# Performance work log

Measured on AMD Instinct MI355X. Metric: run time of the kernel, lower is better.

Reference implementation:

```python
import jax, jax.numpy as jnp
import numpy as np

N_NODES = 100000
N_EDGES = 1600000
N_GRAPHS = 128


def _gru(x, w_ih, w_hh, b_ih, b_hh):
    # x: [N, T, D]; torch nn.GRU single layer, batch_first
    N, T, D = x.shape
    H = w_hh.shape[1]
    gi = jnp.einsum('ntd,gd->ntg', x, w_ih) + b_ih  # [N, T, 3H]

    def step(h, g_t):
        gh = h @ w_hh.T + b_hh
        i_r, i_z, i_n = jnp.split(g_t, 3, axis=-1)
        h_r, h_z, h_n = jnp.split(gh, 3, axis=-1)
        r = jax.nn.sigmoid(i_r + h_r)
        z = jax.nn.sigmoid(i_z + h_z)
        n = jnp.tanh(i_n + r * h_n)
        h_new = (1 - z) * n + z * h
        return h_new, None

    h0 = jnp.zeros((N, H), x.dtype)
    h, _ = jax.lax.scan(step, h0, jnp.swapaxes(gi, 0, 1))
    return h  # [N, H]


def _gat(x, W, att_src, att_dst, bias, src, dst, num_nodes, concat):
    # PyG GATConv: linear, per-head attention logits, segment softmax over dst, scatter-add
    H, C = att_src.shape
    xs = (x @ W).reshape(num_nodes, H, C)
    a_src = (xs * att_src).sum(-1)  # [N, H]
    a_dst = (xs * att_dst).sum(-1)  # [N, H]
    e = jax.nn.leaky_relu(a_src[src] + a_dst[dst], 0.2)  # [E, H]
    emax = jax.ops.segment_max(e, dst, num_segments=num_nodes)
    ee = jnp.exp(e - emax[dst])
    denom = jax.ops.segment_sum(ee, dst, num_segments=num_nodes)
    alpha = ee / (denom[dst] + 1e-16)
    msg = xs[src] * alpha[:, :, None]  # [E, H, C]
    out = jax.ops.segment_sum(msg, dst, num_segments=num_nodes)  # [N, H, C]
    if concat:
        out = out.reshape(num_nodes, H * C)
    else:
        out = out.mean(axis=1)
    return out + bias


def setup_inputs() -> dict:
    key = jax.random.key(0)
    ks = jax.random.split(key, 20)
    s = 0.05
    inp = {
        'x': jax.random.normal(ks[0], (N_NODES, 8, 128), jnp.float32),
        'edge_index': jax.random.randint(ks[1], (2, N_EDGES), 0, N_NODES, jnp.int32),
        'batch': jnp.sort(jax.random.randint(ks[2], (N_NODES,), 0, N_GRAPHS, jnp.int32)),
        'num_graphs': N_GRAPHS,
        'gru_w_ih': jax.random.normal(ks[3], (192, 128)) * s,
        'gru_w_hh': jax.random.normal(ks[4], (192, 64)) * s,
        'gru_b_ih': jax.random.normal(ks[5], (192,)) * s,
        'gru_b_hh': jax.random.normal(ks[6], (192,)) * s,
        'W1': jax.random.normal(ks[7], (64, 256)) * s,
        'att_src1': jax.random.normal(ks[8], (4, 64)) * s,
        'att_dst1': jax.random.normal(ks[9], (4, 64)) * s,
        'b1': jax.random.normal(ks[10], (256,)) * s,
        'W2': jax.random.normal(ks[11], (256, 64)) * s,
        'att_src2': jax.random.normal(ks[12], (1, 64)) * s,
        'att_dst2': jax.random.normal(ks[13], (1, 64)) * s,
        'b2': jax.random.normal(ks[14], (64,)) * s,
        'attn_w': jax.random.normal(ks[15], (64, 1)) * s,
        'attn_b': jax.random.normal(ks[16], (1,)) * s,
        'fc_w': jax.random.normal(ks[17], (64, 10)) * s,
        'fc_b': jax.random.normal(ks[18], (10,)) * s,
    }
    return inp


def reference(x, edge_index, batch, num_graphs, gru_w_ih, gru_w_hh, gru_b_ih, gru_b_hh,
              W1, att_src1, att_dst1, b1, W2, att_src2, att_dst2, b2,
              attn_w, attn_b, fc_w, fc_b):
    N = x.shape[0]
    h = _gru(x, gru_w_ih, gru_w_hh, gru_b_ih, gru_b_hh)  # [N, 64]
    # GATConv default add_self_loops=True
    loops = jnp.arange(N, dtype=edge_index.dtype)
    src = jnp.concatenate([edge_index[0], loops])
    dst = jnp.concatenate([edge_index[1], loops])
    h = jax.nn.relu(_gat(h, W1, att_src1, att_dst1, b1, src, dst, N, concat=True))   # [N, 256]
    h = jax.nn.relu(_gat(h, W2, att_src2, att_dst2, b2, src, dst, N, concat=False))  # [N, 64]
    # softmax over dim=1 of [N,1] -> all ones (faithful to the original code)
    aw = jax.nn.softmax(h @ attn_w + attn_b, axis=1)  # [N, 1]
    weighted = aw * h
    sums = jax.ops.segment_sum(weighted, batch, num_segments=num_graphs)  # [G, 64]
    counts = jax.ops.segment_sum(jnp.ones((N,), h.dtype), batch, num_segments=num_graphs)
    graph_feat = sums / jnp.maximum(counts, 1.0)[:, None]
    out = graph_feat @ fc_w + fc_b
    return jax.nn.log_softmax(out, axis=-1)
```

## Files before the change

kernel.cpp:

```cpp
#include <hip/hip_runtime.h>
#include <stdint.h>


typedef __attribute__((ext_vector_type(8))) short short8;
typedef __attribute__((ext_vector_type(4))) float f32x4;
typedef __attribute__((ext_vector_type(2))) float f32x2;
typedef __attribute__((ext_vector_type(2))) unsigned int u32x2;
typedef __attribute__((ext_vector_type(4))) unsigned int u32x4;

__device__ __forceinline__ unsigned short f2bf(float f) {
    unsigned u = __float_as_uint(f);
    u += 0x7FFFu + ((u >> 16) & 1u);
    return (unsigned short)(u >> 16);
}
__device__ __forceinline__ float bf2f(unsigned short h) {
    return __uint_as_float(((unsigned)h) << 16);
}
__device__ __forceinline__ unsigned cvtpk(float lo, float hi) {
    unsigned r;
    asm("v_cvt_pk_bf16_f32 %0, %1, %2" : "=v"(r) : "v"(lo), "v"(hi));
    return r;
}
__device__ __forceinline__ unsigned short f2bfq(float v) {
    unsigned r;
    asm("v_cvt_pk_bf16_f32 %0, %1, %1" : "=v"(r) : "v"(v));
    return (unsigned short)r;
}
__device__ __forceinline__ float lrelu(float x) { return x > 0.f ? x : 0.2f * x; }
__device__ __forceinline__ float fsig(float a) {
    return __builtin_amdgcn_rcpf(1.f + __expf(-a));
}
__device__ __forceinline__ float ftanh(float a) {
    return 2.f * __builtin_amdgcn_rcpf(1.f + __expf(-2.f * a)) - 1.f;
}
__device__ __forceinline__ unsigned enc4fp8(float a, float b, float c, float d) {
    unsigned r = __builtin_amdgcn_cvt_pk_fp8_f32(a, b, 0, false);
    r = __builtin_amdgcn_cvt_pk_fp8_f32(c, d, r, true);
    return r;
}
__device__ __forceinline__ unsigned char enc1fp8(float v) {
    return (unsigned char)(__builtin_amdgcn_cvt_pk_fp8_f32(v, v, 0, false) & 0xff);
}

__device__ void pack_body(const float* __restrict__ src, unsigned short* __restrict__ dst,
                          int K, int NCOL, int ldsrc, int transposed, int blk, int tid) {
    int id = blk * 256 + tid;
    int KT = K >> 5;
    int nfrag = (NCOL >> 4) * KT;
    if (id >= nfrag * 64) return;
    int l = id & 63;
    int f = id >> 6;
    int kt = f % KT, ct = f / KT;
    int col = ct * 16 + (l & 15);
    int kbase = kt * 32 + ((l >> 4) << 3);
#pragma unroll
    for (int i = 0; i < 8; i++) {
        int k = kbase + i;
        float v = transposed ? src[(size_t)col * ldsrc + k] : src[(size_t)k * ldsrc + col];
        dst[((size_t)f * 64 + l) * 8 + i] = f2bf(v);
    }
}
__device__ void packv_body(const float* __restrict__ W, const float* __restrict__ avs,
                           const float* __restrict__ avd, unsigned short* __restrict__ dst,
                           int K, int H, int ldW, int blk, int tid) {
    int id = blk * 256 + tid;
    int KT = K >> 5;
    if (id >= KT * 64) return;
    int l = id & 63, f = id >> 6;
    int col = l & 15;
    int kbase = f * 32 + ((l >> 4) << 3);
    for (int i = 0; i < 8; i++) {
        int k = kbase + i;
        float val = 0.f;
        if (col < 2 * H) {
            int h = col >> 1;
            const float* av = (col & 1) ? avd : avs;
            for (int c = 0; c < 64; c++) val += W[(size_t)k * ldW + h * 64 + c] * av[h * 64 + c];
        }
        dst[((size_t)f * 64 + l) * 8 + i] = f2bf(val);
    }
}
__global__ void k_prep(const float* w_ih, const float* w_hh, const float* W1, const float* W2,
                       const float* as1, const float* ad1, const float* as2, const float* ad2,
                       const float* b1,
                       unsigned short* p_gi, unsigned short* p_gh,
                       unsigned short* p_w1, unsigned short* p_w2,
                       unsigned short* p_v1, unsigned short* p_v2,
                       float* b1p) {
    int b = blockIdx.x, tid = threadIdx.x;
    if (b < 12)      pack_body(w_ih, p_gi, 128, 192, 128, 1, b, tid);
    else if (b < 18) pack_body(w_hh, p_gh, 64, 192, 64, 1, b - 12, tid);
    else if (b < 26) pack_body(W1, p_w1, 64, 256, 256, 0, b - 18, tid);
    else if (b < 34) pack_body(W2, p_w2, 256, 64, 64, 0, b - 26, tid);
    else if (b < 35) packv_body(W1, as1, ad1, p_v1, 64, 4, 256, b - 34, tid);
    else if (b < 37) packv_body(W2, as2, ad2, p_v2, 256, 1, 64, b - 35, tid);
    else {
        int o = tid;
        int p = (o & 0xC0) | ((o & 15) << 2) | ((o >> 4) & 3);
        b1p[p] = b1[o];
    }
}

__launch_bounds__(256, 2)
__global__ void k_gru(const float* __restrict__ x,
                      const unsigned short* __restrict__ pgi,
                      const unsigned short* __restrict__ pgh,
                      const float* __restrict__ b_ih, const float* __restrict__ b_hh,
                      unsigned short* __restrict__ h1, int N) {
    __shared__ unsigned short x_pack[4 * 4 * 64 * 8];
    __shared__ unsigned short h_pack[4 * 2 * 64 * 8];

    const int tid = threadIdx.x;
    const int w = tid >> 6;
    const int l = tid & 63;
    const int row0 = blockIdx.x * 64;

    short8 wgi[3][4], wgh[3][2];
#pragma unroll
    for (int g = 0; g < 3; g++) {
        int ctg = g * 4 + w;
#pragma unroll
        for (int kt = 0; kt < 4; kt++)
            wgi[g][kt] = *(const short8*)(pgi + ((size_t)(ctg * 4 + kt) * 64 + l) * 8);
#pragma unroll
        for (int kt = 0; kt < 2; kt++)
            wgh[g][kt] = *(const short8*)(pgh + ((size_t)(ctg * 2 + kt) * 64 + l) * 8);
    }
    const int j = (w << 4) + (l & 15);
    const float bs_r = b_ih[j] + b_hh[j];
    const float bs_z = b_ih[64 + j] + b_hh[64 + j];
    const float bi_n = b_ih[128 + j], bh_n = b_hh[128 + j];

    f32x4 hreg[4];
    const f32x4 z4 = {0.f, 0.f, 0.f, 0.f};
#pragma unroll
    for (int m = 0; m < 4; m++) hreg[m] = z4;

    const int sr = tid >> 2, sub = tid & 3;
    const int snode = min(row0 + sr, N - 1);
    const int slane = (sr & 15) | (sub << 4);
    const int sm = sr >> 4;
    const float* xbase = x + (size_t)snode * 1024;

    float4 pre[8];
#pragma unroll
    for (int it = 0; it < 4; it++) {
        int d0 = it * 32 + sub * 8;
        pre[2 * it] = *(const float4*)(xbase + d0);
        pre[2 * it + 1] = *(const float4*)(xbase + d0 + 4);
    }

    for (int t = 0; t < 8; t++) {
        u32x4 pk[4];
#pragma unroll
        for (int it = 0; it < 4; it++) {
            float4 va = pre[2 * it], vb = pre[2 * it + 1];
            u32x4 p;
            p[0] = cvtpk(va.x, va.y); p[1] = cvtpk(va.z, va.w);
            p[2] = cvtpk(vb.x, vb.y); p[3] = cvtpk(vb.z, vb.w);
            pk[it] = p;
        }
        if (t > 0) {
#pragma unroll
            for (int m = 0; m < 4; m++)
#pragma unroll
                for (int q = 0; q < 4; q++) {
                    int rl = ((l >> 4) << 2) + q;
                    int lane2 = rl | (((j >> 3) & 3) << 4);
                    h_pack[((m * 2 + (j >> 5)) * 64 + lane2) * 8 + (j & 7)] = f2bfq(hreg[m][q]);
                }
        }
#pragma unroll
        for (int it = 0; it < 4; it++)
            *(u32x4*)&x_pack[((sm * 4 + it) * 64 + slane) * 8] = pk[it];
        __syncthreads();

        if (t < 7) {
            const float* xp = xbase + (t + 1) * 128;
#pragma unroll
            for (int it = 0; it < 4; it++) {
                int d0 = it * 32 + sub * 8;
                pre[2 * it] = *(const float4*)(xp + d0);
                pre[2 * it + 1] = *(const float4*)(xp + d0 + 4);
            }
        }

        f32x4 agi[4][3], aghn[4];
#pragma unroll
        for (int m = 0; m < 4; m++) {
            agi[m][0] = z4; agi[m][1] = z4; agi[m][2] = z4; aghn[m] = z4;
        }

#pragma unroll
        for (int m = 0; m < 4; m++) {
#pragma unroll
            for (int kt = 0; kt < 4; kt++) {
                short8 a = *(const short8*)&x_pack[((m * 4 + kt) * 64 + l) * 8];
#pragma unroll
                for (int g = 0; g < 3; g++)
                    agi[m][g] = __builtin_amdgcn_mfma_f32_16x16x32_bf16(a, wgi[g][kt], agi[m][g], 0, 0, 0);
            }
            if (t > 0) {
#pragma unroll
                for (int kt = 0; kt < 2; kt++) {
                    short8 a = *(const short8*)&h_pack[((m * 2 + kt) * 64 + l) * 8];
                    agi[m][0] = __builtin_amdgcn_mfma_f32_16x16x32_bf16(a, wgh[0][kt], agi[m][0], 0, 0, 0);
                    agi[m][1] = __builtin_amdgcn_mfma_f32_16x16x32_bf16(a, wgh[1][kt], agi[m][1], 0, 0, 0);
                    aghn[m]   = __builtin_amdgcn_mfma_f32_16x16x32_bf16(a, wgh[2][kt], aghn[m], 0, 0, 0);
                }
            }
        }
#pragma unroll
        for (int m = 0; m < 4; m++) {
#pragma unroll
            for (int q = 0; q < 4; q++) {
                float rr = fsig(agi[m][0][q] + bs_r);
                float zz = fsig(agi[m][1][q] + bs_z);
                float hn = aghn[m][q] + bh_n;
                float nn = ftanh(agi[m][2][q] + bi_n + rr * hn);
                hreg[m][q] = nn + zz * (hreg[m][q] - nn);
            }
        }
        __syncthreads();
    }
#pragma unroll
    for (int m = 0; m < 4; m++)
#pragma unroll
        for (int q = 0; q < 4; q++) {
            int node = row0 + (m << 4) + ((l >> 4) << 2) + q;
            if (node < N) h1[(size_t)node * 64 + j] = f2bfq(hreg[m][q]);
        }
}

__launch_bounds__(256, 2)
__global__ void k_gemm1(const unsigned short* __restrict__ A,
                        const unsigned short* __restrict__ packB,
                        const unsigned short* __restrict__ pv1,
                        unsigned char* __restrict__ Cf,
                        float* __restrict__ aS, float* __restrict__ aD, int N) {
    constexpr int KT = 2, CPW = 4;
    __shared__ unsigned short a_pack[4 * KT * 64 * 8];

    const int tid = threadIdx.x, w = tid >> 6, l = tid & 63;
    const int row0 = blockIdx.x * 64;

    short8 bf[CPW][KT];
#pragma unroll
    for (int ci = 0; ci < CPW; ci++)
#pragma unroll
        for (int kt = 0; kt < KT; kt++)
            bf[ci][kt] = *(const short8*)(packB + ((size_t)((w * CPW + ci) * KT + kt) * 64 + l) * 8);

    const int sr = tid >> 2, sub = tid & 3;
    const int snode = min(row0 + sr, N - 1);
    const unsigned short* ap = A + (size_t)snode * 64;
#pragma unroll
    for (int it = 0; it < KT; it++) {
        int d0 = it * 32 + sub * 8;
        short8 v = *(const short8*)(ap + d0);
        *(short8*)&a_pack[(((sr >> 4) * KT + it) * 64 + ((sr & 15) | (sub << 4))) * 8] = v;
    }
    __syncthreads();

    const f32x4 z4 = {0.f, 0.f, 0.f, 0.f};
    f32x4 acc[4][CPW];
#pragma unroll
    for (int m = 0; m < 4; m++)
#pragma unroll
        for (int ci = 0; ci < CPW; ci++) acc[m][ci] = z4;

#pragma unroll
    for (int m = 0; m < 4; m++)
#pragma unroll
        for (int kt = 0; kt < KT; kt++) {
            short8 a = *(const short8*)&a_pack[((m * KT + kt) * 64 + l) * 8];
#pragma unroll
            for (int ci = 0; ci < CPW; ci++)
                acc[m][ci] = __builtin_amdgcn_mfma_f32_16x16x32_bf16(a, bf[ci][kt], acc[m][ci], 0, 0, 0);
        }

    f32x4 acce = z4;
#pragma unroll
    for (int kt = 0; kt < KT; kt++) {
        short8 be = *(const short8*)(pv1 + ((size_t)kt * 64 + l) * 8);
        short8 a = *(const short8*)&a_pack[((w * KT + kt) * 64 + l) * 8];
        acce = __builtin_amdgcn_mfma_f32_16x16x32_bf16(a, be, acce, 0, 0, 0);
    }
    int colE = l & 15;
    if (colE < 8) {
        int h = colE >> 1;
#pragma unroll
        for (int q = 0; q < 4; q++) {
            int node = row0 + (w << 4) + ((l >> 4) << 2) + q;
            if (node < N) {
                if (colE & 1) aD[node * 4 + h] = acce[q];
                else          aS[node * 4 + h] = acce[q];
            }
        }
    }

    const int lc = l & 15;
#pragma unroll
    for (int m = 0; m < 4; m++)
#pragma unroll
        for (int q = 0; q < 4; q++) {
            int node = row0 + (m << 4) + ((l >> 4) << 2) + q;
            if (node < N) {
                unsigned d = enc4fp8(acc[m][0][q], acc[m][1][q], acc[m][2][q], acc[m][3][q]);
                *(unsigned*)(Cf + (size_t)node * 256 + w * 64 + lc * 4) = d;
            }
        }
}

__launch_bounds__(256, 2)
__global__ void k_gemm2(const unsigned short* __restrict__ A,
                        const unsigned short* __restrict__ packB,
                        const unsigned short* __restrict__ pv2,
                        unsigned char* __restrict__ Cf,
                        float* __restrict__ aS, float* __restrict__ aD, int N) {
    constexpr int KT = 8;
    __shared__ unsigned short a_pack[4 * KT * 64 * 8];

    const int tid = threadIdx.x, w = tid >> 6, l = tid & 63;
    const int row0 = blockIdx.x * 64;

    short8 bf[KT];
#pragma unroll
    for (int kt = 0; kt < KT; kt++)
        bf[kt] = *(const short8*)(packB + ((size_t)(w * KT + kt) * 64 + l) * 8);

    const int sr = tid >> 2, sub = tid & 3;
    const int snode = min(row0 + sr, N - 1);
    const unsigned short* ap = A + (size_t)snode * 256;
#pragma unroll
    for (int it = 0; it < KT; it++) {
        int d0 = it * 32 + sub * 8;
        short8 v = *(const short8*)(ap + d0);
        *(short8*)&a_pack[(((sr >> 4) * KT + it) * 64 + ((sr & 15) | (sub << 4))) * 8] = v;
    }
    __syncthreads();

    const f32x4 z4 = {0.f, 0.f, 0.f, 0.f};
    f32x4 acc[4];
#pragma unroll
    for (int m = 0; m < 4; m++) acc[m] = z4;

#pragma unroll
    for (int m = 0; m < 4; m++)
#pragma unroll
        for (int kt = 0; kt < KT; kt++) {
            short8 a = *(const short8*)&a_pack[((m * KT + kt) * 64 + l) * 8];
            acc[m] = __builtin_amdgcn_mfma_f32_16x16x32_bf16(a, bf[kt], acc[m], 0, 0, 0);
        }

    f32x4 acce = z4;
#pragma unroll
    for (int kt = 0; kt < KT; kt++) {
        short8 be = *(const short8*)(pv2 + ((size_t)kt * 64 + l) * 8);
        short8 a = *(const short8*)&a_pack[((w * KT + kt) * 64 + l) * 8];
        acce = __builtin_amdgcn_mfma_f32_16x16x32_bf16(a, be, acce, 0, 0, 0);
    }
    int colE = l & 15;
    if (colE < 2) {
#pragma unroll
        for (int q = 0; q < 4; q++) {
            int node = row0 + (w << 4) + ((l >> 4) << 2) + q;
            if (node < N) {
                if (colE) aD[node] = acce[q];
                else      aS[node] = acce[q];
            }
        }
    }

    int colw = w * 16 + (l & 15);
#pragma unroll
    for (int m = 0; m < 4; m++)
#pragma unroll
        for (int q = 0; q < 4; q++) {
            int node = row0 + (m << 4) + ((l >> 4) << 2) + q;
            if (node < N) Cf[(size_t)node * 64 + colw] = enc1fp8(acc[m][q]);
        }
}

__global__ void k_deg(const int* __restrict__ dst, int* __restrict__ deg, int E) {
    int i = blockIdx.x * blockDim.x + threadIdx.x;
    if (i < E) atomicAdd(&deg[dst[i]], 1);
}
__global__ void k_scan1(const int* __restrict__ deg, int* __restrict__ inc,
                        int* __restrict__ bsum, int N) {
    __shared__ int wsum[16];
    int tid = threadIdx.x;
    int i = blockIdx.x * 1024 + tid;
    int v = (i < N) ? deg[i] : 0;
    int lane = tid & 63, wv = tid >> 6;
    int s = v;
#pragma unroll
    for (int d = 1; d < 64; d <<= 1) {
        int t = __shfl_up(s, d);
        if (lane >= d) s += t;
    }
    if (lane == 63) wsum[wv] = s;
    __syncthreads();
    if (tid == 0) {
        int run = 0;
#pragma unroll
        for (int k = 0; k < 16; k++) { int t = wsum[k]; wsum[k] = run; run += t; }
        bsum[blockIdx.x] = run;
    }
    __syncthreads();
    s += wsum[wv];
    if (i < N) inc[i] = s;
}
__global__ void k_scan2(int* __restrict__ bsum, int nb) {
    __shared__ int w0tot;
    int tid = threadIdx.x;
    int v = (tid < nb) ? bsum[tid] : 0;
    int lane = tid & 63, wv = tid >> 6;
    int s = v;
#pragma unroll
    for (int d = 1; d < 64; d <<= 1) {
        int t = __shfl_up(s, d);
        if (lane >= d) s += t;
    }
    if (tid == 63) w0tot = s;
    __syncthreads();
    int ex = s - v + (wv ? w0tot : 0);
    if (tid < nb) bsum[tid] = ex;
}
__global__ void k_scan3(const int* __restrict__ inc, const int* __restrict__ bsum,
                        int* __restrict__ off, int* __restrict__ cursor, int N) {
    int i = blockIdx.x * blockDim.x + threadIdx.x;
    if (i < N) { off[i + 1] = inc[i] + bsum[i >> 10]; cursor[i] = 0; }
    if (i == 0) off[0] = 0;
}
__global__ void k_fill(const int* __restrict__ srcv, const int* __restrict__ dstv,
                       const int* __restrict__ off, int* __restrict__ cursor,
                       int* __restrict__ ssrc, int E) {
    int i = blockIdx.x * blockDim.x + threadIdx.x;
    if (i < E) {
        int d = dstv[i];
        int pos = off[d] + atomicAdd(&cursor[d], 1);
        ssrc[pos] = srcv[i];
    }
}

__global__ void k_agg1(const unsigned char* __restrict__ xs,
                       const float* __restrict__ a_s, const float* __restrict__ a_d,
                       const int* __restrict__ off, const int* __restrict__ ssrc,
                       const float* __restrict__ b1p,
                       unsigned short* __restrict__ out, int N) {
    int v = blockIdx.x * 4 + (threadIdx.x >> 6);
    if (v >= N) return;
    const int l = threadIdx.x & 63;
    const int eq = l >> 4;
    const int cq = l & 15;
    const int H = cq >> 2;
    const float adv = a_d[v * 4 + H];
    const int beg = off[v], end = off[v + 1];
    const int cnt = end - beg;

    float s_;
    float ac[16];
    {
        u32x4 xv = *(const u32x4*)(xs + (size_t)v * 256 + cq * 16);
        float pv = (eq == 0) ? __expf(lrelu(a_s[v * 4 + H] + adv)) : 0.f;
        s_ = pv;
#pragma unroll
        for (int wd = 0; wd < 4; wd++) {
            f32x2 lo = __builtin_amdgcn_cvt_pk_f32_fp8(xv[wd], false);
            f32x2 hi = __builtin_amdgcn_cvt_pk_f32_fp8(xv[wd], true);
            ac[wd * 4 + 0] = pv * lo[0]; ac[wd * 4 + 1] = pv * lo[1];
            ac[wd * 4 + 2] = pv * hi[0]; ac[wd * 4 + 3] = pv * hi[1];
        }
    }

#define AG1_LOAD(S, POS) { int pp = min((POS) + eq, cl); int uu = ssrc[beg + pp]; \
        aa##S = a_s[uu * 4 + H]; x##S = *(const u32x4*)(xs + (size_t)uu * 256 + cq * 16); }
#define AG1_PROC(S) { float p = __expf(lrelu(aa##S + adv)); s_ += p; \
        _Pragma("unroll") for (int wd = 0; wd < 4; wd++) { \
            f32x2 lo = __builtin_amdgcn_cvt_pk_f32_fp8(x##S[wd], false); \
            f32x2 hi = __builtin_amdgcn_cvt_pk_f32_fp8(x##S[wd], true); \
            ac[wd * 4 + 0] += p * lo[0]; ac[wd * 4 + 1] += p * lo[1]; \
            ac[wd * 4 + 2] += p * hi[0]; ac[wd * 4 + 3] += p * hi[1]; } }

    float aa0 = 0.f, aa1 = 0.f, aa2 = 0.f;
    u32x4 x0 = {0, 0, 0, 0}, x1 = {0, 0, 0, 0}, x2 = {0, 0, 0, 0};
    int k = 0;
    if (cnt > 0) {
        const int cl = cnt - 1;
        AG1_LOAD(0, 0) AG1_LOAD(1, 4) AG1_LOAD(2, 8)
        for (; k + 12 <= cnt; k += 12) {
            AG1_PROC(0) AG1_LOAD(0, k + 12)
            AG1_PROC(1) AG1_LOAD(1, k + 16)
            AG1_PROC(2) AG1_LOAD(2, k + 20)
        }
        if (k + eq < cnt)     AG1_PROC(0)
        if (k + 4 + eq < cnt) AG1_PROC(1)
        if (k + 8 + eq < cnt) AG1_PROC(2)
    }
#undef AG1_LOAD
#undef AG1_PROC

#pragma unroll
    for (int msk = 16; msk < 64; msk <<= 1) {
        s_ += __shfl_xor(s_, msk);
#pragma unroll
        for (int i = 0; i < 16; i++) ac[i] += __shfl_xor(ac[i], msk);
    }

    if (eq == 0) {
        float inv = __builtin_amdgcn_rcpf(s_ + 1e-16f);
        float bp[16];
#pragma unroll
        for (int i = 0; i < 4; i++)
            *(float4*)&bp[i * 4] = *(const float4*)(b1p + cq * 16 + i * 4);
#pragma unroll
        for (int b = 0; b < 4; b++) {
            float r0 = fmaxf(ac[b]      * inv + bp[b],      0.f);
            float r1 = fmaxf(ac[4 + b]  * inv + bp[4 + b],  0.f);
            float r2 = fmaxf(ac[8 + b]  * inv + bp[8 + b],  0.f);
            float r3 = fmaxf(ac[12 + b] * inv + bp[12 + b], 0.f);
            u32x2 o;
            o[0] = cvtpk(r0, r1); o[1] = cvtpk(r2, r3);
            *(u32x2*)(out + (size_t)v * 256 + H * 64 + b * 16 + (cq & 3) * 4) = o;
        }
    }
}

__global__ void k_agg2(const unsigned char* __restrict__ xs,
                       const float* __restrict__ a_s, const float* __restrict__ a_d,
                       const int* __restrict__ off, const int* __restrict__ ssrc,
                       const float* __restrict__ bias,
                       float* __restrict__ out, int N) {
    int v = blockIdx.x * 4 + (threadIdx.x >> 6);
    if (v >= N) return;
    const int l = threadIdx.x & 63;
    const int eo = l >> 3;
    const int cq = l & 7;
    const int c0 = cq * 8;
    const float adv = a_d[v];
    const int beg = off[v], end = off[v + 1];
    const int cnt = end - beg;

    float s_;
    float ac[8];
    {
        u32x2 xv = *(const u32x2*)(xs + (size_t)v * 64 + c0);
        float pv = (eo == 0) ? __expf(lrelu(a_s[v] + adv)) : 0.f;
        s_ = pv;
#pragma unroll
        for (int wd = 0; wd < 2; wd++) {
            f32x2 lo = __builtin_amdgcn_cvt_pk_f32_fp8(xv[wd], false);
            f32x2 hi = __builtin_amdgcn_cvt_pk_f32_fp8(xv[wd], true);
            ac[wd * 4 + 0] = pv * lo[0]; ac[wd * 4 + 1] = pv * lo[1];
            ac[wd * 4 + 2] = pv * hi[0]; ac[wd * 4 + 3] = pv * hi[1];
        }
    }

#define AG2_LOAD(S, POS) { int pp = min((POS) + eo, cl); int uu = ssrc[beg + pp]; \
        aa##S = a_s[uu]; x##S = *(const u32x2*)(xs + (size_t)uu * 64 + c0); }
#define AG2_PROC(S) { float p = __expf(lrelu(aa##S + adv)); s_ += p; \
        _Pragma("unroll") for (int wd = 0; wd < 2; wd++) { \
            f32x2 lo = __builtin_amdgcn_cvt_pk_f32_fp8(x##S[wd], false); \
            f32x2 hi = __builtin_amdgcn_cvt_pk_f32_fp8(x##S[wd], true); \
            ac[wd * 4 + 0] += p * lo[0]; ac[wd * 4 + 1] += p * lo[1]; \
            ac[wd * 4 + 2] += p * hi[0]; ac[wd * 4 + 3] += p * hi[1]; } }

    float aa0 = 0.f, aa1 = 0.f;
    u32x2 x0 = {0, 0}, x1 = {0, 0};
    int k = 0;
    if (cnt > 0) {
        const int cl = cnt - 1;
        AG2_LOAD(0, 0) AG2_LOAD(1, 8)
        for (; k + 16 <= cnt; k += 16) {
            AG2_PROC(0) AG2_LOAD(0, k + 16)
            AG2_PROC(1) AG2_LOAD(1, k + 24)
        }
        if (k + eo < cnt)     AG2_PROC(0)
        if (k + 8 + eo < cnt) AG2_PROC(1)
    }
#undef AG2_LOAD
#undef AG2_PROC

#pragma unroll
    for (int msk = 8; msk < 64; msk <<= 1) {
        s_ += __shfl_xor(s_, msk);
#pragma unroll
        for (int i = 0; i < 8; i++) ac[i] += __shfl_xor(ac[i], msk);
    }
    if (eo == 0) {
        float inv = __builtin_amdgcn_rcpf(s_ + 1e-16f);
        float4 b4a = *(const float4*)(bias + c0);
        float4 b4b = *(const float4*)(bias + c0 + 4);
        float4 o1, o2;
        o1.x = fmaxf(ac[0] * inv + b4a.x, 0.f);
        o1.y = fmaxf(ac[1] * inv + b4a.y, 0.f);
        o1.z = fmaxf(ac[2] * inv + b4a.z, 0.f);
        o1.w = fmaxf(ac[3] * inv + b4a.w, 0.f);
        o2.x = fmaxf(ac[4] * inv + b4b.x, 0.f);
        o2.y = fmaxf(ac[5] * inv + b4b.y, 0.f);
        o2.z = fmaxf(ac[6] * inv + b4b.z, 0.f);
        o2.w = fmaxf(ac[7] * inv + b4b.w, 0.f);
        *(float4*)(out + (size_t)v * 64 + c0) = o1;
        *(float4*)(out + (size_t)v * 64 + c0 + 4) = o2;
    }
}

__global__ void k_pool(const float* __restrict__ h3, const int* __restrict__ batch,
                       const float* __restrict__ fc_w, const float* __restrict__ fc_b,
                       float* __restrict__ out, int N, int G) {
    __shared__ float red[4][64];
    __shared__ float meanv[64];
    __shared__ float lg[10];
    int g = blockIdx.x;
    int tid = threadIdx.x, c = tid & 63, ro = tid >> 6;
    int lo = 0, hi = N;
    while (lo < hi) { int mid = (lo + hi) >> 1; if (batch[mid] < g) lo = mid + 1; else hi = mid; }
    int s0 = lo;
    lo = 0; hi = N;
    while (lo < hi) { int mid = (lo + hi) >> 1; if (batch[mid] < g + 1) lo = mid + 1; else hi = mid; }
    int s1 = lo;
    float p = 0.f;
    for (int r = s0 + ro; r < s1; r += 4) p += h3[(size_t)r * 64 + c];
    red[ro][c] = p;
    __syncthreads();
    if (tid < 64) {
        float tot = red[0][c] + red[1][c] + red[2][c] + red[3][c];
        float cnt = (float)max(s1 - s0, 1);
        meanv[c] = tot / cnt;
    }
    __syncthreads();
    if (tid < 10) {
        float lv = fc_b[tid];
        for (int k = 0; k < 64; k++) lv += meanv[k] * fc_w[k * 10 + tid];
        lg[tid] = lv;
    }
    __syncthreads();
    if (tid == 0) {
        float mxv = lg[0];
        for (int k = 1; k < 10; k++) mxv = fmaxf(mxv, lg[k]);
        float ss = 0.f;
        for (int k = 0; k < 10; k++) ss += expf(lg[k] - mxv);
        float lse = mxv + logf(ss);
        for (int k = 0; k < 10; k++) out[g * 10 + k] = lg[k] - lse;
    }
}

extern "C" void kernel_launch(void* const* d_in, const int* in_sizes, int n_in,
                              void* d_out, int out_size, void* d_ws, size_t ws_size,
                              hipStream_t stream) {
    const float* x = (const float*)d_in[0];
    const int* ei = (const int*)d_in[1];
    const int* batch = (const int*)d_in[2];
    const float* w_ih = (const float*)d_in[4];
    const float* w_hh = (const float*)d_in[5];
    const float* b_ih = (const float*)d_in[6];
    const float* b_hh = (const float*)d_in[7];
    const float* W1 = (const float*)d_in[8];
    const float* as1 = (const float*)d_in[9];
    const float* ad1 = (const float*)d_in[10];
    const float* b1 = (const float*)d_in[11];
    const float* W2 = (const float*)d_in[12];
    const float* as2 = (const float*)d_in[13];
    const float* ad2 = (const float*)d_in[14];
    const float* b2 = (const float*)d_in[15];
    const float* fc_w = (const float*)d_in[18];
    const float* fc_b = (const float*)d_in[19];
    float* out = (float*)d_out;

    const int N = in_sizes[0] / (8 * 128);
    const int E = in_sizes[1] / 2;
    const int G = 128;

    char* ws = (char*)d_ws;
    size_t cur = 0;
    auto alloc = [&](size_t b) { size_t r = cur; cur += (b + 255) & ~(size_t)255; return r; };
    unsigned short* p_gi = (unsigned short*)(ws + alloc((size_t)12 * 4 * 64 * 8 * 2));
    unsigned short* p_gh = (unsigned short*)(ws + alloc((size_t)12 * 2 * 64 * 8 * 2));
    unsigned short* p_w1 = (unsigned short*)(ws + alloc((size_t)16 * 2 * 64 * 8 * 2));
    unsigned short* p_w2 = (unsigned short*)(ws + alloc((size_t)4 * 8 * 64 * 8 * 2));
    unsigned short* p_v1 = (unsigned short*)(ws + alloc((size_t)2 * 64 * 8 * 2));
    unsigned short* p_v2 = (unsigned short*)(ws + alloc((size_t)8 * 64 * 8 * 2));
    float* b1p = (float*)(ws + alloc((size_t)256 * 4));
    unsigned short* h1 = (unsigned short*)(ws + alloc((size_t)N * 64 * 2));
    unsigned char* xs1f = (unsigned char*)(ws + alloc((size_t)N * 256));
    unsigned short* h2 = (unsigned short*)(ws + alloc((size_t)N * 256 * 2));
    float* h3 = (float*)(ws + alloc((size_t)N * 64 * 4));
    float* aS = (float*)(ws + alloc((size_t)N * 4 * 4));
    float* aD = (float*)(ws + alloc((size_t)N * 4 * 4));
    int* deg = (int*)(ws + alloc((size_t)N * 4));
    int* offp = (int*)(ws + alloc((size_t)(N + 1) * 4));
    int* inc = (int*)(ws + alloc((size_t)N * 4));
    int* bsum = (int*)(ws + alloc((size_t)128 * 4));
    int* ssrc = (int*)(ws + alloc((size_t)E * 4));

    k_prep<<<38, 256, 0, stream>>>(w_ih, w_hh, W1, W2, as1, ad1, as2, ad2, b1,
                                   p_gi, p_gh, p_w1, p_w2, p_v1, p_v2, b1p);

    const int nbscan = (N + 1023) / 1024;
    hipMemsetAsync(deg, 0, (size_t)N * 4, stream);
    k_deg<<<(E + 255) / 256, 256, 0, stream>>>(ei + E, deg, E);
    k_scan1<<<nbscan, 1024, 0, stream>>>(deg, inc, bsum, N);
    k_scan2<<<1, 128, 0, stream>>>(bsum, nbscan);
    k_scan3<<<(N + 255) / 256, 256, 0, stream>>>(inc, bsum, offp, deg , N);
    k_fill<<<(E + 255) / 256, 256, 0, stream>>>(ei, ei + E, offp, deg, ssrc, E);

    const int nb64 = (N + 63) / 64;
    const int nb4 = (N + 3) / 4;

    k_gru<<<nb64, 256, 0, stream>>>(x, p_gi, p_gh, b_ih, b_hh, h1, N);

    k_gemm1<<<nb64, 256, 0, stream>>>(h1, p_w1, p_v1, xs1f, aS, aD, N);
    k_agg1<<<nb4, 256, 0, stream>>>(xs1f, aS, aD, offp, ssrc, b1p, h2, N);

    k_gemm2<<<nb64, 256, 0, stream>>>(h2, p_w2, p_v2, xs1f , aS, aD, N);
    k_agg2<<<nb4, 256, 0, stream>>>(xs1f, aS, aD, offp, ssrc, b2, h3, N);

    k_pool<<<G, 256, 0, stream>>>(h3, batch, fc_w, fc_b, out, N, G);
}
```

Baseline: 481.1 us.

## Fuse GRU with GEMM1 and GAT aggregation 1 with GEMM2, fold memset into prep

Merges the GRU kernel with the first GAT linear projection so the hidden state goes straight from registers through LDS into the MFMA GEMM instead of being written to and re-read from global memory. The first aggregation is fused with the second projection: each wave aggregates 16 nodes serially into an LDS tile, then the block runs GEMM2 on it, which removes the N×256 bf16 h2 round trip. The degree memset moves into extra k_prep blocks. In exchange, agg1 drops from 4 waves per node to a serial per-wave loop over 16 nodes, which reduces latency hiding on the irregular gather, and the GRU launch bound changes to 4 blocks per SIMD, which may push registers into spills.

```diff
diff --git a/kernel.cpp b/kernel.cpp
--- a/kernel.cpp
+++ b/kernel.cpp
@@ -86,8 +86,13 @@
                        unsigned short* p_gi, unsigned short* p_gh,
                        unsigned short* p_w1, unsigned short* p_w2,
                        unsigned short* p_v1, unsigned short* p_v2,
-                       float* b1p) {
+                       float* b1p, int* deg, int N) {
     int b = blockIdx.x, tid = threadIdx.x;
+    if (b >= 38) {
+        int i = (b - 38) * 256 + tid;
+        if (i < N) deg[i] = 0;
+        return;
+    }
     if (b < 12)      pack_body(w_ih, p_gi, 128, 192, 128, 1, b, tid);
     else if (b < 18) pack_body(w_hh, p_gh, 64, 192, 64, 1, b - 12, tid);
     else if (b < 26) pack_body(W1, p_w1, 64, 256, 256, 0, b - 18, tid);
@@ -101,12 +106,15 @@
     }
 }
 
-__launch_bounds__(256, 2)
-__global__ void k_gru(const float* __restrict__ x,
-                      const unsigned short* __restrict__ pgi,
-                      const unsigned short* __restrict__ pgh,
-                      const float* __restrict__ b_ih, const float* __restrict__ b_hh,
-                      unsigned short* __restrict__ h1, int N) {
+__launch_bounds__(256, 4)
+__global__ void k_gru_gemm1(const float* __restrict__ x,
+                            const unsigned short* __restrict__ pgi,
+                            const unsigned short* __restrict__ pgh,
+                            const float* __restrict__ b_ih, const float* __restrict__ b_hh,
+                            const unsigned short* __restrict__ packB,
+                            const unsigned short* __restrict__ pv1,
+                            unsigned char* __restrict__ Cf,
+                            float* __restrict__ aS, float* __restrict__ aD, int N) {
     __shared__ unsigned short x_pack[4 * 4 * 64 * 8];
     __shared__ unsigned short h_pack[4 * 2 * 64 * 8];
 
@@ -223,68 +231,49 @@
         }
         __syncthreads();
     }
+
+    short8 bfw[4][2];
+#pragma unroll
+    for (int ci = 0; ci < 4; ci++)
+#pragma unroll
+        for (int kt = 0; kt < 2; kt++)
+            bfw[ci][kt] = *(const short8*)(packB + ((size_t)((w * 4 + ci) * 2 + kt) * 64 + l) * 8);
+    short8 bev[2];
+#pragma unroll
+    for (int kt = 0; kt < 2; kt++)
+        bev[kt] = *(const short8*)(pv1 + ((size_t)kt * 64 + l) * 8);
+
 #pragma unroll
     for (int m = 0; m < 4; m++)
 #pragma unroll
         for (int q = 0; q < 4; q++) {
-            int node = row0 + (m << 4) + ((l >> 4) << 2) + q;
-            if (node < N) h1[(size_t)node * 64 + j] = f2bfq(hreg[m][q]);
-        }
-}
-
-__launch_bounds__(256, 2)
-__global__ void k_gemm1(const unsigned short* __restrict__ A,
-                        const unsigned short* __restrict__ packB,
-                        const unsigned short* __restrict__ pv1,
-                        unsigned char* __restrict__ Cf,
-                        float* __restrict__ aS, float* __restrict__ aD, int N) {
-    constexpr int KT = 2, CPW = 4;
-    __shared__ unsigned short a_pack[4 * KT * 64 * 8];
-
-    const int tid = threadIdx.x, w = tid >> 6, l = tid & 63;
-    const int row0 = blockIdx.x * 64;
-
-    short8 bf[CPW][KT];
-#pragma unroll
-    for (int ci = 0; ci < CPW; ci++)
-#pragma unroll
-        for (int kt = 0; kt < KT; kt++)
-            bf[ci][kt] = *(const short8*)(packB + ((size_t)((w * CPW + ci) * KT + kt) * 64 + l) * 8);
-
-    const int sr = tid >> 2, sub = tid & 3;
-    const int snode = min(row0 + sr, N - 1);
-    const unsigned short* ap = A + (size_t)snode * 64;
-#pragma unroll
-    for (int it = 0; it < KT; it++) {
-        int d0 = it * 32 + sub * 8;
-        short8 v = *(const short8*)(ap + d0);
-        *(short8*)&a_pack[(((sr >> 4) * KT + it) * 64 + ((sr & 15) | (sub << 4))) * 8] = v;
-    }
-    __syncthreads();
-
-    const f32x4 z4 = {0.f, 0.f, 0.f, 0.f};
-    f32x4 acc[4][CPW];
+            int rl = ((l >> 4) << 2) + q;
+            int lane2 = rl | (((j >> 3) & 3) << 4);
+            h_pack[((m * 2 + (j >> 5)) * 64 + lane2) * 8 + (j & 7)] = f2bfq(hreg[m][q]);
+        }
+    __syncthreads();
+
+    f32x4 acc[4][4];
 #pragma unroll
     for (int m = 0; m < 4; m++)
 #pragma unroll
-        for (int ci = 0; ci < CPW; ci++) acc[m][ci] = z4;
+        for (int ci = 0; ci < 4; ci++) acc[m][ci] = z4;
 
 #pragma unroll
     for (int m = 0; m < 4; m++)
 #pragma unroll
-        for (int kt = 0; kt < KT; kt++) {
-            short8 a = *(const short8*)&a_pack[((m * KT + kt) * 64 + l) * 8];
-#pragma unroll
-            for (int ci = 0; ci < CPW; ci++)
-                acc[m][ci] = __builtin_amdgcn_mfma_f32_16x16x32_bf16(a, bf[ci][kt], acc[m][ci], 0, 0, 0);
+        for (int kt = 0; kt < 2; kt++) {
+            short8 a = *(const short8*)&h_pack[((m * 2 + kt) * 64 + l) * 8];
+#pragma unroll
+            for (int ci = 0; ci < 4; ci++)
+                acc[m][ci] = __builtin_amdgcn_mfma_f32_16x16x32_bf16(a, bfw[ci][kt], acc[m][ci], 0, 0, 0);
         }
 
     f32x4 acce = z4;
 #pragma unroll
-    for (int kt = 0; kt < KT; kt++) {
-        short8 be = *(const short8*)(pv1 + ((size_t)kt * 64 + l) * 8);
-        short8 a = *(const short8*)&a_pack[((w * KT + kt) * 64 + l) * 8];
-        acce = __builtin_amdgcn_mfma_f32_16x16x32_bf16(a, be, acce, 0, 0, 0);
+    for (int kt = 0; kt < 2; kt++) {
+        short8 a = *(const short8*)&h_pack[((w * 2 + kt) * 64 + l) * 8];
+        acce = __builtin_amdgcn_mfma_f32_16x16x32_bf16(a, bev[kt], acce, 0, 0, 0);
     }
     int colE = l & 15;
     if (colE < 8) {
@@ -298,7 +287,6 @@
             }
         }
     }
-
     const int lc = l & 15;
 #pragma unroll
     for (int m = 0; m < 4; m++)
@@ -309,76 +297,6 @@
                 unsigned d = enc4fp8(acc[m][0][q], acc[m][1][q], acc[m][2][q], acc[m][3][q]);
                 *(unsigned*)(Cf + (size_t)node * 256 + w * 64 + lc * 4) = d;
             }
-        }
-}
-
-__launch_bounds__(256, 2)
-__global__ void k_gemm2(const unsigned short* __restrict__ A,
-                        const unsigned short* __restrict__ packB,
-                        const unsigned short* __restrict__ pv2,
-                        unsigned char* __restrict__ Cf,
-                        float* __restrict__ aS, float* __restrict__ aD, int N) {
-    constexpr int KT = 8;
-    __shared__ unsigned short a_pack[4 * KT * 64 * 8];
-
-    const int tid = threadIdx.x, w = tid >> 6, l = tid & 63;
-    const int row0 = blockIdx.x * 64;
-
-    short8 bf[KT];
-#pragma unroll
-    for (int kt = 0; kt < KT; kt++)
-        bf[kt] = *(const short8*)(packB + ((size_t)(w * KT + kt) * 64 + l) * 8);
-
-    const int sr = tid >> 2, sub = tid & 3;
-    const int snode = min(row0 + sr, N - 1);
-    const unsigned short* ap = A + (size_t)snode * 256;
-#pragma unroll
-    for (int it = 0; it < KT; it++) {
-        int d0 = it * 32 + sub * 8;
-        short8 v = *(const short8*)(ap + d0);
-        *(short8*)&a_pack[(((sr >> 4) * KT + it) * 64 + ((sr & 15) | (sub << 4))) * 8] = v;
-    }
-    __syncthreads();
-
-    const f32x4 z4 = {0.f, 0.f, 0.f, 0.f};
-    f32x4 acc[4];
-#pragma unroll
-    for (int m = 0; m < 4; m++) acc[m] = z4;
-
-#pragma unroll
-    for (int m = 0; m < 4; m++)
-#pragma unroll
-        for (int kt = 0; kt < KT; kt++) {
-            short8 a = *(const short8*)&a_pack[((m * KT + kt) * 64 + l) * 8];
-            acc[m] = __builtin_amdgcn_mfma_f32_16x16x32_bf16(a, bf[kt], acc[m], 0, 0, 0);
-        }
-
-    f32x4 acce = z4;
-#pragma unroll
-    for (int kt = 0; kt < KT; kt++) {
-        short8 be = *(const short8*)(pv2 + ((size_t)kt * 64 + l) * 8);
-        short8 a = *(const short8*)&a_pack[((w * KT + kt) * 64 + l) * 8];
-        acce = __builtin_amdgcn_mfma_f32_16x16x32_bf16(a, be, acce, 0, 0, 0);
-    }
-    int colE = l & 15;
-    if (colE < 2) {
-#pragma unroll
-        for (int q = 0; q < 4; q++) {
-            int node = row0 + (w << 4) + ((l >> 4) << 2) + q;
-            if (node < N) {
-                if (colE) aD[node] = acce[q];
-                else      aS[node] = acce[q];
-            }
-        }
-    }
-
-    int colw = w * 16 + (l & 15);
-#pragma unroll
-    for (int m = 0; m < 4; m++)
-#pragma unroll
-        for (int q = 0; q < 4; q++) {
-            int node = row0 + (m << 4) + ((l >> 4) << 2) + q;
-            if (node < N) Cf[(size_t)node * 64 + colw] = enc1fp8(acc[m][q]);
         }
 }
 
@@ -444,35 +362,48 @@
     }
 }
 
-__global__ void k_agg1(const unsigned char* __restrict__ xs,
-                       const float* __restrict__ a_s, const float* __restrict__ a_d,
-                       const int* __restrict__ off, const int* __restrict__ ssrc,
-                       const float* __restrict__ b1p,
-                       unsigned short* __restrict__ out, int N) {
-    int v = blockIdx.x * 4 + (threadIdx.x >> 6);
-    if (v >= N) return;
-    const int l = threadIdx.x & 63;
+__global__ void k_agg1_gemm2(const unsigned char* __restrict__ xs,
+                             const float* __restrict__ a_s, const float* __restrict__ a_d,
+                             const int* __restrict__ off, const int* __restrict__ ssrc,
+                             const float* __restrict__ b1p,
+                             const unsigned short* __restrict__ packB2,
+                             const unsigned short* __restrict__ pv2,
+                             unsigned char* __restrict__ Cf,
+                             float* __restrict__ aS2, float* __restrict__ aD2, int N) {
+    __shared__ unsigned short h2t[4 * 8 * 64 * 8];
+
+    const int tid = threadIdx.x, w = tid >> 6, l = tid & 63;
+    const int row0 = blockIdx.x * 64;
     const int eq = l >> 4;
     const int cq = l & 15;
     const int H = cq >> 2;
-    const float adv = a_d[v * 4 + H];
-    const int beg = off[v], end = off[v + 1];
-    const int cnt = end - beg;
-
-    float s_;
-    float ac[16];
-    {
-        u32x4 xv = *(const u32x4*)(xs + (size_t)v * 256 + cq * 16);
-        float pv = (eq == 0) ? __expf(lrelu(a_s[v * 4 + H] + adv)) : 0.f;
-        s_ = pv;
-#pragma unroll
-        for (int wd = 0; wd < 4; wd++) {
-            f32x2 lo = __builtin_amdgcn_cvt_pk_f32_fp8(xv[wd], false);
-            f32x2 hi = __builtin_amdgcn_cvt_pk_f32_fp8(xv[wd], true);
-            ac[wd * 4 + 0] = pv * lo[0]; ac[wd * 4 + 1] = pv * lo[1];
-            ac[wd * 4 + 2] = pv * hi[0]; ac[wd * 4 + 3] = pv * hi[1];
-        }
-    }
+
+    float bp[16];
+#pragma unroll
+    for (int i = 0; i < 4; i++)
+        *(float4*)&bp[i * 4] = *(const float4*)(b1p + cq * 16 + i * 4);
+
+    for (int i = 0; i < 16; i++) {
+        const int v = row0 + w * 16 + i;
+        const int vv = min(v, N - 1);
+        const float adv = a_d[vv * 4 + H];
+        const int beg = off[vv], end = off[vv + 1];
+        const int cnt = (v < N) ? (end - beg) : 0;
+
+        float s_;
+        float ac[16];
+        {
+            u32x4 xv = *(const u32x4*)(xs + (size_t)vv * 256 + cq * 16);
+            float pv = (eq == 0) ? __expf(lrelu(a_s[vv * 4 + H] + adv)) : 0.f;
+            s_ = pv;
+#pragma unroll
+            for (int wd = 0; wd < 4; wd++) {
+                f32x2 lo = __builtin_amdgcn_cvt_pk_f32_fp8(xv[wd], false);
+                f32x2 hi = __builtin_amdgcn_cvt_pk_f32_fp8(xv[wd], true);
+                ac[wd * 4 + 0] = pv * lo[0]; ac[wd * 4 + 1] = pv * lo[1];
+                ac[wd * 4 + 2] = pv * hi[0]; ac[wd * 4 + 3] = pv * hi[1];
+            }
+        }
 
 #define AG1_LOAD(S, POS) { int pp = min((POS) + eq, cl); int uu = ssrc[beg + pp]; \
         aa##S = a_s[uu * 4 + H]; x##S = *(const u32x4*)(xs + (size_t)uu * 256 + cq * 16); }
@@ -483,48 +414,93 @@
             ac[wd * 4 + 0] += p * lo[0]; ac[wd * 4 + 1] += p * lo[1]; \
             ac[wd * 4 + 2] += p * hi[0]; ac[wd * 4 + 3] += p * hi[1]; } }
 
-    float aa0 = 0.f, aa1 = 0.f, aa2 = 0.f;
-    u32x4 x0 = {0, 0, 0, 0}, x1 = {0, 0, 0, 0}, x2 = {0, 0, 0, 0};
-    int k = 0;
-    if (cnt > 0) {
-        const int cl = cnt - 1;
-        AG1_LOAD(0, 0) AG1_LOAD(1, 4) AG1_LOAD(2, 8)
-        for (; k + 12 <= cnt; k += 12) {
-            AG1_PROC(0) AG1_LOAD(0, k + 12)
-            AG1_PROC(1) AG1_LOAD(1, k + 16)
-            AG1_PROC(2) AG1_LOAD(2, k + 20)
-        }
-        if (k + eq < cnt)     AG1_PROC(0)
-        if (k + 4 + eq < cnt) AG1_PROC(1)
-        if (k + 8 + eq < cnt) AG1_PROC(2)
-    }
+        float aa0 = 0.f, aa1 = 0.f, aa2 = 0.f;
+        u32x4 x0 = {0, 0, 0, 0}, x1 = {0, 0, 0, 0}, x2 = {0, 0, 0, 0};
+        int k = 0;
+        if (cnt > 0) {
+            const int cl = cnt - 1;
+            AG1_LOAD(0, 0) AG1_LOAD(1, 4) AG1_LOAD(2, 8)
+            for (; k + 12 <= cnt; k += 12) {
+                AG1_PROC(0) AG1_LOAD(0, k + 12)
+                AG1_PROC(1) AG1_LOAD(1, k + 16)
+                AG1_PROC(2) AG1_LOAD(2, k + 20)
+            }
+            if (k + eq < cnt)     AG1_PROC(0)
+            if (k + 4 + eq < cnt) AG1_PROC(1)
+            if (k + 8 + eq < cnt) AG1_PROC(2)
+        }
 #undef AG1_LOAD
 #undef AG1_PROC
 
 #pragma unroll
-    for (int msk = 16; msk < 64; msk <<= 1) {
-        s_ += __shfl_xor(s_, msk);
-#pragma unroll
-        for (int i = 0; i < 16; i++) ac[i] += __shfl_xor(ac[i], msk);
-    }
-
-    if (eq == 0) {
-        float inv = __builtin_amdgcn_rcpf(s_ + 1e-16f);
-        float bp[16];
-#pragma unroll
-        for (int i = 0; i < 4; i++)
-            *(float4*)&bp[i * 4] = *(const float4*)(b1p + cq * 16 + i * 4);
-#pragma unroll
-        for (int b = 0; b < 4; b++) {
-            float r0 = fmaxf(ac[b]      * inv + bp[b],      0.f);
-            float r1 = fmaxf(ac[4 + b]  * inv + bp[4 + b],  0.f);
-            float r2 = fmaxf(ac[8 + b]  * inv + bp[8 + b],  0.f);
-            float r3 = fmaxf(ac[12 + b] * inv + bp[12 + b], 0.f);
-            u32x2 o;
-            o[0] = cvtpk(r0, r1); o[1] = cvtpk(r2, r3);
-            *(u32x2*)(out + (size_t)v * 256 + H * 64 + b * 16 + (cq & 3) * 4) = o;
-        }
-    }
+        for (int msk = 16; msk < 64; msk <<= 1) {
+            s_ += __shfl_xor(s_, msk);
+#pragma unroll
+            for (int t = 0; t < 16; t++) ac[t] += __shfl_xor(ac[t], msk);
+        }
+
+        if (l < 16) {
+            float inv = __builtin_amdgcn_rcpf(s_ + 1e-16f);
+#pragma unroll
+            for (int b = 0; b < 4; b++) {
+                float r0 = fmaxf(ac[b]      * inv + bp[b],      0.f);
+                float r1 = fmaxf(ac[4 + b]  * inv + bp[4 + b],  0.f);
+                float r2 = fmaxf(ac[8 + b]  * inv + bp[8 + b],  0.f);
+                float r3 = fmaxf(ac[12 + b] * inv + bp[12 + b], 0.f);
+                int c = H * 64 + b * 16 + (cq & 3) * 4;
+                int kt = c >> 5, sb = (c >> 3) & 3, io = c & 7;
+                u32x2 o;
+                o[0] = cvtpk(r0, r1); o[1] = cvtpk(r2, r3);
+                *(u32x2*)&h2t[(((w * 8 + kt) * 64) + (i | (sb << 4))) * 8 + io] = o;
+            }
+        }
+    }
+    __syncthreads();
+
+    short8 bf2[8];
+#pragma unroll
+    for (int kt = 0; kt < 8; kt++)
+        bf2[kt] = *(const short8*)(packB2 + ((size_t)(w * 8 + kt) * 64 + l) * 8);
+
+    const f32x4 z4 = {0.f, 0.f, 0.f, 0.f};
+    f32x4 acc[4];
+#pragma unroll
+    for (int m = 0; m < 4; m++) acc[m] = z4;
+
+#pragma unroll
+    for (int m = 0; m < 4; m++)
+#pragma unroll
+        for (int kt = 0; kt < 8; kt++) {
+            short8 a = *(const short8*)&h2t[((m * 8 + kt) * 64 + l) * 8];
+            acc[m] = __builtin_amdgcn_mfma_f32_16x16x32_bf16(a, bf2[kt], acc[m], 0, 0, 0);
+        }
+
+    f32x4 acce = z4;
+#pragma unroll
+    for (int kt = 0; kt < 8; kt++) {
+        short8 be = *(const short8*)(pv2 + ((size_t)kt * 64 + l) * 8);
+        short8 a = *(const short8*)&h2t[((w * 8 + kt) * 64 + l) * 8];
+        acce = __builtin_amdgcn_mfma_f32_16x16x32_bf16(a, be, acce, 0, 0, 0);
+    }
+    int colE = l & 15;
+    if (colE < 2) {
+#pragma unroll
+        for (int q = 0; q < 4; q++) {
+            int node = row0 + (w << 4) + ((l >> 4) << 2) + q;
+            if (node < N) {
+                if (colE) aD2[node] = acce[q];
+                else      aS2[node] = acce[q];
+            }
+        }
+    }
+    int colw = w * 16 + (l & 15);
+#pragma unroll
+    for (int m = 0; m < 4; m++)
+#pragma unroll
+        for (int q = 0; q < 4; q++) {
+            int node = row0 + (m << 4) + ((l >> 4) << 2) + q;
+            if (node < N) Cf[(size_t)node * 64 + colw] = enc1fp8(acc[m][q]);
+        }
 }
 
 __global__ void k_agg2(const unsigned char* __restrict__ xs,
@@ -682,39 +658,40 @@
     unsigned short* p_v1 = (unsigned short*)(ws + alloc((size_t)2 * 64 * 8 * 2));
     unsigned short* p_v2 = (unsigned short*)(ws + alloc((size_t)8 * 64 * 8 * 2));
     float* b1p = (float*)(ws + alloc((size_t)256 * 4));
-    unsigned short* h1 = (unsigned short*)(ws + alloc((size_t)N * 64 * 2));
     unsigned char* xs1f = (unsigned char*)(ws + alloc((size_t)N * 256));
-    unsigned short* h2 = (unsigned short*)(ws + alloc((size_t)N * 256 * 2));
+    unsigned char* xs2f = (unsigned char*)(ws + alloc((size_t)N * 64));
     float* h3 = (float*)(ws + alloc((size_t)N * 64 * 4));
     float* aS = (float*)(ws + alloc((size_t)N * 4 * 4));
     float* aD = (float*)(ws + alloc((size_t)N * 4 * 4));
+    float* aS2 = (float*)(ws + alloc((size_t)N * 4));
+    float* aD2 = (float*)(ws + alloc((size_t)N * 4));
     int* deg = (int*)(ws + alloc((size_t)N * 4));
     int* offp = (int*)(ws + alloc((size_t)(N + 1) * 4));
     int* inc = (int*)(ws + alloc((size_t)N * 4));
     int* bsum = (int*)(ws + alloc((size_t)128 * 4));
     int* ssrc = (int*)(ws + alloc((size_t)E * 4));
 
-    k_prep<<<38, 256, 0, stream>>>(w_ih, w_hh, W1, W2, as1, ad1, as2, ad2, b1,
-                                   p_gi, p_gh, p_w1, p_w2, p_v1, p_v2, b1p);
-
+    const int nb64 = (N + 63) / 64;
+    const int nb4 = (N + 3) / 4;
     const int nbscan = (N + 1023) / 1024;
-    hipMemsetAsync(deg, 0, (size_t)N * 4, stream);
+
+    k_prep<<<38 + (N + 255) / 256, 256, 0, stream>>>(
+        w_ih, w_hh, W1, W2, as1, ad1, as2, ad2, b1,
+        p_gi, p_gh, p_w1, p_w2, p_v1, p_v2, b1p, deg, N);
+
     k_deg<<<(E + 255) / 256, 256, 0, stream>>>(ei + E, deg, E);
     k_scan1<<<nbscan, 1024, 0, stream>>>(deg, inc, bsum, N);
     k_scan2<<<1, 128, 0, stream>>>(bsum, nbscan);
     k_scan3<<<(N + 255) / 256, 256, 0, stream>>>(inc, bsum, offp, deg , N);
     k_fill<<<(E + 255) / 256, 256, 0, stream>>>(ei, ei + E, offp, deg, ssrc, E);
 
-    const int nb64 = (N + 63) / 64;
-    const int nb4 = (N + 3) / 4;
-
-    k_gru<<<nb64, 256, 0, stream>>>(x, p_gi, p_gh, b_ih, b_hh, h1, N);
-
-    k_gemm1<<<nb64, 256, 0, stream>>>(h1, p_w1, p_v1, xs1f, aS, aD, N);
-    k_agg1<<<nb4, 256, 0, stream>>>(xs1f, aS, aD, offp, ssrc, b1p, h2, N);
-
-    k_gemm2<<<nb64, 256, 0, stream>>>(h2, p_w2, p_v2, xs1f , aS, aD, N);
-    k_agg2<<<nb4, 256, 0, stream>>>(xs1f, aS, aD, offp, ssrc, b2, h3, N);
+    k_gru_gemm1<<<nb64, 256, 0, stream>>>(x, p_gi, p_gh, b_ih, b_hh,
+                                          p_w1, p_v1, xs1f, aS, aD, N);
+
+    k_agg1_gemm2<<<nb64, 256, 0, stream>>>(xs1f, aS, aD, offp, ssrc, b1p,
+                                           p_w2, p_v2, xs2f, aS2, aD2, N);
+
+    k_agg2<<<nb4, 256, 0, stream>>>(xs2f, aS2, aD2, offp, ssrc, b2, h3, N);
 
     k_pool<<<G, 256, 0, stream>>>(h3, batch, fc_w, fc_b, out, N, G);
 }
```

Result: slower. 850.1 us (+76.7%).
